# Performance work log

Hardware: AMD Instinct MI355X
Metric: run time of the kernel (lower is better)

The kernel has to match this reference:

```python
import jax, jax.numpy as jnp
import numpy as np

N_EMBD = 1024
NUM_HEADS = 16
HEAD_SIZE = 64


def setup_inputs() -> dict:
    key = jax.random.key(0)
    ks = jax.random.split(key, 6)
    B, T, C, hs = 2, 2048, N_EMBD, HEAD_SIZE
    s = 0.02
    return {
        "x": jax.random.normal(ks[0], (B, T, C), dtype=jnp.float32),
        "Wk": jax.random.normal(ks[1], (hs, C), dtype=jnp.float32) * s,  # torch Linear weight [out,in]
        "Wv": jax.random.normal(ks[2], (hs, C), dtype=jnp.float32) * s,
        "Wq": jax.random.normal(ks[3], (C, C), dtype=jnp.float32) * s,
        "Wp": jax.random.normal(ks[4], (C, C), dtype=jnp.float32) * s,
        "bp": jax.random.normal(ks[5], (C,), dtype=jnp.float32) * s,
    }


def reference(x, Wk, Wv, Wq, Wp, bp):
    B, T, C = x.shape
    H, hs = NUM_HEADS, HEAD_SIZE
    k = x @ Wk.T                      # [B,T,hs]
    v = x @ Wv.T                      # [B,T,hs]
    q = x @ Wq.T                      # [B,T,C]
    # Faithful to torch: raw view of [B,T,C] -> [B,H,T,hs] (row-major reshape, not transpose)
    q = q.reshape(B, H, T, hs)
    k = k.reshape(B, 1, T, hs)
    v = v.reshape(B, 1, T, hs)
    att = jnp.einsum("bhqd,bhkd->bhqk", q, jnp.broadcast_to(k, (B, 1, T, hs))) * (hs ** -0.5)
    mask = jnp.tril(jnp.ones((T, T), dtype=bool))[None, None]  # [1,1,T,T]
    att = jnp.where(mask, att, -jnp.inf)
    att = jax.nn.softmax(att, axis=-1)
    y = jnp.einsum("bhqk,bhkd->bhqd", att, jnp.broadcast_to(v, (B, 1, T, hs)))  # [B,H,T,hs]
    y = jnp.transpose(y, (0, 2, 1, 3)).reshape(B, T, C)
    return y @ Wp.T + bp
```

## Files before the change

kernel.cpp:

```cpp
#include <hip/hip_runtime.h>
#include <cstddef>
#include <cstdint>

#define B_N 2
#define T_N 2048
#define C_N 1024
#define H_N 16
#define HS_N 64
#define M_N (B_N * T_N)

typedef __attribute__((ext_vector_type(8))) short bf16x8;
typedef __attribute__((ext_vector_type(4))) float f32x4;

#define QSCALE 0.18033688011112042f

__device__ __forceinline__ ushort f2bf(float f) {
    union { float f; uint32_t u; } v; v.f = f;
    uint32_t r = v.u + 0x7fffu + ((v.u >> 16) & 1u);
    return (ushort)(r >> 16);
}

#define GLL16(g, l)                                                         \
    __builtin_amdgcn_global_load_lds(                                       \
        (const __attribute__((address_space(1))) unsigned int*)(g),         \
        (__attribute__((address_space(3))) unsigned int*)(l), 16, 0, 0)

__global__ void cvt_all_kernel(const float* __restrict__ x,
                               const float* __restrict__ Wq,
                               const float* __restrict__ Wp,
                               const float* __restrict__ Wk,
                               const float* __restrict__ Wv,
                               ushort* __restrict__ xb,
                               ushort* __restrict__ Wqb,
                               ushort* __restrict__ Wpb,
                               ushort* __restrict__ Wkvb) {
    const int S0 = M_N * C_N / 4;
    const int S1 = S0 + C_N * C_N / 4;
    const int S2 = S1 + C_N * C_N / 4;
    const int S3 = S2 + HS_N * C_N / 4;
    const int S4 = S3 + HS_N * C_N / 4;
    const int stride = gridDim.x * blockDim.x;
    for (int i = blockIdx.x * blockDim.x + threadIdx.x; i < S4; i += stride) {
        const float* src; ushort* dst; int j; float sc = 1.f;
        if (i < S0)      { src = x;  dst = xb;   j = i; }
        else if (i < S1) { src = Wq; dst = Wqb;  j = i - S0; sc = QSCALE; }
        else if (i < S2) { src = Wp; dst = Wpb;  j = i - S1; }
        else if (i < S3) { src = Wk; dst = Wkvb; j = i - S2; }
        else             { src = Wv; dst = Wkvb + HS_N * C_N; j = i - S3; }
        const float4 f = ((const float4*)src)[j];
        ushort4 o;
        o.x = f2bf(f.x * sc); o.y = f2bf(f.y * sc);
        o.z = f2bf(f.z * sc); o.w = f2bf(f.w * sc);
        ((ushort4*)dst)[j] = o;
    }
}

template <int MODE>
__global__ __launch_bounds__(256, 2) void gemm_bf16(
    const ushort* __restrict__ A,
    const ushort* __restrict__ W,
    const float* __restrict__ bias,
    void* __restrict__ Cout,
    ushort* __restrict__ kb,
    ushort* __restrict__ vbt,
    int K)
{
    __shared__ ushort As[64 * 64];
    __shared__ ushort Bs[128 * 64];
    const int m0 = blockIdx.x * 64;
    const int n0 = blockIdx.y * 128;
    const int tid = threadIdx.x;
    const int wid = tid >> 6;
    const int lane = tid & 63;
    const int ln = lane & 15;
    const int quad = lane >> 4;
    const int wm = wid >> 1, wn = wid & 1;

    f32x4 acc[2][4];
    #pragma unroll
    for (int i = 0; i < 2; ++i)
        #pragma unroll
        for (int j = 0; j < 4; ++j)
            acc[i][j] = (f32x4){0.f, 0.f, 0.f, 0.f};

    const int srow = lane >> 3;
    const int schk = (lane & 7) ^ srow;

    for (int k0 = 0; k0 < K; k0 += 64) {
        __syncthreads();
        #pragma unroll
        for (int t = 0; t < 2; ++t) {
            const int seg = wid * 2 + t;
            GLL16(A + (size_t)(m0 + seg * 8 + srow) * K + k0 + schk * 8,
                  As + seg * 512);
        }
        #pragma unroll
        for (int t = 0; t < 4; ++t) {
            const int seg = wid * 4 + t;
            GLL16(W + (size_t)(n0 + seg * 8 + srow) * K + k0 + schk * 8,
                  Bs + seg * 512);
        }
        __syncthreads();

        #pragma unroll
        for (int hh = 0; hh < 2; ++hh) {
            bf16x8 af[2], bf[4];
            const int sw = ln & 7;
            #pragma unroll
            for (int i = 0; i < 2; ++i) {
                const int row = wm * 32 + i * 16 + ln;
                af[i] = *(const bf16x8*)&As[row * 64 + (((hh * 4 + quad) ^ sw) * 8)];
            }
            #pragma unroll
            for (int j = 0; j < 4; ++j) {
                const int row = wn * 64 + j * 16 + ln;
                bf[j] = *(const bf16x8*)&Bs[row * 64 + (((hh * 4 + quad) ^ sw) * 8)];
            }
            #pragma unroll
            for (int i = 0; i < 2; ++i)
                #pragma unroll
                for (int j = 0; j < 4; ++j)
                    acc[i][j] = __builtin_amdgcn_mfma_f32_16x16x32_bf16(
                        af[i], bf[j], acc[i][j], 0, 0, 0);
        }
    }

    if (MODE == 1 && n0 >= C_N) {
        #pragma unroll
        for (int i = 0; i < 2; ++i) {
            const int row0 = m0 + wm * 32 + i * 16 + quad * 4;
            #pragma unroll
            for (int j = 0; j < 4; ++j) {
                const int c2 = wn * 64 + j * 16 + ln;
                if (c2 >= 64) {
                    const int d = c2 - 64;
                    const int b = row0 >> 11;
                    const int t0 = row0 & 2047;
                    ushort4 pk;
                    pk.x = f2bf(acc[i][j][0]); pk.y = f2bf(acc[i][j][1]);
                    pk.z = f2bf(acc[i][j][2]); pk.w = f2bf(acc[i][j][3]);
                    *(ushort4*)&vbt[((size_t)b * 64 + d) * T_N + t0] = pk;
                } else {
                    #pragma unroll
                    for (int reg = 0; reg < 4; ++reg)
                        kb[(size_t)(row0 + reg) * 64 + c2] = f2bf(acc[i][j][reg]);
                }
            }
        }
        return;
    }

    #pragma unroll
    for (int i = 0; i < 2; ++i) {
        #pragma unroll
        for (int j = 0; j < 4; ++j) {
            const int col = n0 + wn * 64 + j * 16 + ln;
            const float bv = (MODE == 0) ? bias[col] : 0.f;
            #pragma unroll
            for (int reg = 0; reg < 4; ++reg) {
                const int row = m0 + wm * 32 + i * 16 + quad * 4 + reg;
                const float v = acc[i][j][reg] + bv;
                if (MODE == 0)
                    ((float*)Cout)[(size_t)row * C_N + col] = v;
                else
                    ((ushort*)Cout)[(size_t)row * C_N + col] = f2bf(v);
            }
        }
    }
}

__global__ __launch_bounds__(256, 2) void attn_mfma_kernel(
    const ushort* __restrict__ qb,
    const ushort* __restrict__ kb,
    const ushort* __restrict__ vbt,
    ushort* __restrict__ yb)
{
    __shared__ ushort Ks[2][64][72];
    __shared__ ushort Vt[2][64][72];
    __shared__ ushort Ps[4][16][72];

    const int bh = blockIdx.x;
    const int b = bh >> 4, h = bh & 15;
    const int p = blockIdx.y;
    const int qA0 = p * 64;
    const int qB0 = (31 - p) * 64;
    const int tid = threadIdx.x;
    const int wid = tid >> 6;
    const int lane = tid & 63;
    const int ln = lane & 15;
    const int quad = lane >> 4;

    const ushort* qstrip = qb + (size_t)b * T_N * C_N + (size_t)h * T_N * HS_N;
    const size_t rB = (size_t)(qB0 + wid * 16 + ln) * HS_N;
    const size_t rA = (size_t)(qA0 + wid * 16 + ln) * HS_N;
    bf16x8 qfB[2], qfA[2];
    qfB[0] = *(const bf16x8*)(qstrip + rB + quad * 8);
    qfB[1] = *(const bf16x8*)(qstrip + rB + 32 + quad * 8);
    qfA[0] = *(const bf16x8*)(qstrip + rA + quad * 8);
    qfA[1] = *(const bf16x8*)(qstrip + rA + 32 + quad * 8);

    f32x4 oB[4], oA[4];
    float lB = 0.f, lA = 0.f;
    #pragma unroll
    for (int nt = 0; nt < 4; ++nt) {
        oB[nt] = (f32x4){0.f, 0.f, 0.f, 0.f};
        oA[nt] = (f32x4){0.f, 0.f, 0.f, 0.f};
    }

    const ushort* kbase = kb + (size_t)b * T_N * HS_N;
    const ushort* vtbase = vbt + (size_t)b * HS_N * T_N;
    const int rs = tid >> 3;
    const int cs = tid & 7;

    const int nkt = 32 - p;

    int4 kc0, kc1, vc0, vc1;
    {
        kc0 = *(const int4*)(kbase + (size_t)rs * HS_N + cs * 8);
        kc1 = *(const int4*)(kbase + (size_t)(rs + 32) * HS_N + cs * 8);
        vc0 = *(const int4*)(vtbase + (size_t)rs * T_N + cs * 8);
        vc1 = *(const int4*)(vtbase + (size_t)(rs + 32) * T_N + cs * 8);
        *(int4*)&Ks[0][rs][cs * 8] = kc0;
        *(int4*)&Ks[0][rs + 32][cs * 8] = kc1;
        *(int4*)&Vt[0][rs][cs * 8] = vc0;
        *(int4*)&Vt[0][rs + 32][cs * 8] = vc1;
    }
    if (nkt > 1) {
        kc0 = *(const int4*)(kbase + (size_t)(64 + rs) * HS_N + cs * 8);
        kc1 = *(const int4*)(kbase + (size_t)(64 + rs + 32) * HS_N + cs * 8);
        vc0 = *(const int4*)(vtbase + (size_t)rs * T_N + 64 + cs * 8);
        vc1 = *(const int4*)(vtbase + (size_t)(rs + 32) * T_N + 64 + cs * 8);
    }
    __syncthreads();

    bf16x8 kf[4][2], vf[4][2];

    auto tile_compute = [&](const bf16x8* qf, f32x4* o, float& l,
                            int qt0, int k0) {
        const int qs0 = qt0 + wid * 16;
        const int qg = qs0 + ln;
        f32x4 sc[4];
        #pragma unroll
        for (int nt = 0; nt < 4; ++nt) {
            sc[nt] = (f32x4){0.f, 0.f, 0.f, 0.f};
            sc[nt] = __builtin_amdgcn_mfma_f32_16x16x32_bf16(
                kf[nt][0], qf[0], sc[nt], 0, 0, 0);
            sc[nt] = __builtin_amdgcn_mfma_f32_16x16x32_bf16(
                kf[nt][1], qf[1], sc[nt], 0, 0, 0);
        }
        const bool dg = (k0 + 63 > qs0);
        #pragma unroll
        for (int nt = 0; nt < 4; ++nt) {
            ushort pk[4];
            #pragma unroll
            for (int reg = 0; reg < 4; ++reg) {
                const int key = k0 + nt * 16 + quad * 4 + reg;
                float sv = sc[nt][reg];
                if (dg && key > qg) sv = -1e30f;
                const float pe = __builtin_amdgcn_exp2f(sv);
                l += pe;
                pk[reg] = f2bf(pe);
            }
            *(uint2*)&Ps[wid][ln][nt * 16 + quad * 4] = *(const uint2*)pk;
        }
        #pragma unroll
        for (int ks2 = 0; ks2 < 2; ++ks2) {
            const bf16x8 pf = *(const bf16x8*)&Ps[wid][ln][ks2 * 32 + quad * 8];
            #pragma unroll
            for (int nt = 0; nt < 4; ++nt)
                o[nt] = __builtin_amdgcn_mfma_f32_16x16x32_bf16(
                    pf, vf[nt][ks2], o[nt], 0, 0, 0);
        }
    };

    for (int kt = 0; kt < nkt; ++kt) {
        const int k0 = kt * 64;
        const int cur = kt & 1, nxt = cur ^ 1;
        if (kt + 1 < nkt) {
            *(int4*)&Ks[nxt][rs][cs * 8] = kc0;
            *(int4*)&Ks[nxt][rs + 32][cs * 8] = kc1;
            *(int4*)&Vt[nxt][rs][cs * 8] = vc0;
            *(int4*)&Vt[nxt][rs + 32][cs * 8] = vc1;
        }
        if (kt + 2 < nkt) {
            const int kn = k0 + 128;
            kc0 = *(const int4*)(kbase + (size_t)(kn + rs) * HS_N + cs * 8);
            kc1 = *(const int4*)(kbase + (size_t)(kn + rs + 32) * HS_N + cs * 8);
            vc0 = *(const int4*)(vtbase + (size_t)rs * T_N + kn + cs * 8);
            vc1 = *(const int4*)(vtbase + (size_t)(rs + 32) * T_N + kn + cs * 8);
        }
        #pragma unroll
        for (int nt = 0; nt < 4; ++nt) {
            kf[nt][0] = *(const bf16x8*)&Ks[cur][nt * 16 + ln][quad * 8];
            kf[nt][1] = *(const bf16x8*)&Ks[cur][nt * 16 + ln][32 + quad * 8];
            vf[nt][0] = *(const bf16x8*)&Vt[cur][nt * 16 + ln][quad * 8];
            vf[nt][1] = *(const bf16x8*)&Vt[cur][nt * 16 + ln][32 + quad * 8];
        }
        tile_compute(qfB, oB, lB, qB0, k0);
        if (kt <= p)
            tile_compute(qfA, oA, lA, qA0, k0);
        __syncthreads();
    }

    #pragma unroll
    for (int t = 0; t < 2; ++t) {
        float l = t ? lA : lB;
        const f32x4* o = t ? oA : oB;
        const int qt0 = t ? qA0 : qB0;
        l += __shfl_xor(l, 16);
        l += __shfl_xor(l, 32);
        #pragma unroll
        for (int reg = 0; reg < 4; ++reg) {
            const float inv = 1.0f / __shfl(l, quad * 4 + reg);
            const int qg = qt0 + wid * 16 + quad * 4 + reg;
            ushort* yrow = yb + (size_t)b * T_N * C_N + (size_t)qg * C_N
                           + h * HS_N;
            #pragma unroll
            for (int nt = 0; nt < 4; ++nt)
                yrow[nt * 16 + ln] = f2bf(o[nt][reg] * inv);
        }
    }
}

extern "C" void kernel_launch(void* const* d_in, const int* in_sizes, int n_in,
                              void* d_out, int out_size, void* d_ws, size_t ws_size,
                              hipStream_t stream) {
    const float* x  = (const float*)d_in[0];
    const float* Wk = (const float*)d_in[1];
    const float* Wv = (const float*)d_in[2];
    const float* Wq = (const float*)d_in[3];
    const float* Wp = (const float*)d_in[4];
    const float* bp = (const float*)d_in[5];
    float* out = (float*)d_out;

    ushort* xb   = (ushort*)d_ws;
    ushort* qb   = xb   + (size_t)M_N * C_N;
    ushort* yb   = qb   + (size_t)M_N * C_N;
    ushort* kbw  = yb   + (size_t)M_N * C_N;
    ushort* vbt  = kbw  + (size_t)M_N * HS_N;
    ushort* Wqb  = vbt  + (size_t)B_N * HS_N * T_N;
    ushort* Wkvb = Wqb  + (size_t)C_N * C_N;
    ushort* Wpb  = Wkvb + (size_t)128 * C_N;

    cvt_all_kernel<<<1024, 256, 0, stream>>>(x, Wq, Wp, Wk, Wv,
                                             xb, Wqb, Wpb, Wkvb);

    gemm_bf16<1><<<dim3(M_N / 64, (C_N + 128) / 128), 256, 0, stream>>>(
        xb, Wqb, nullptr, qb, kbw, vbt, C_N);

    attn_mfma_kernel<<<dim3(B_N * H_N, 16), 256, 0, stream>>>(qb, kbw, vbt, yb);

    gemm_bf16<0><<<dim3(M_N / 64, C_N / 128), 256, 0, stream>>>(
        yb, Wpb, bp, out, nullptr, nullptr, C_N);
}
```

Baseline: 155.1 us.

## Load GEMM and attention MFMA fragments directly from global memory, dropping LDS staging

New measurement: 296.0 us. 90.9% more time.

```diff
diff --git a/kernel.cpp b/kernel.cpp
--- a/kernel.cpp
+++ b/kernel.cpp
@@ -19,11 +19,6 @@
     uint32_t r = v.u + 0x7fffu + ((v.u >> 16) & 1u);
     return (ushort)(r >> 16);
 }
-
-#define GLL16(g, l)                                                         \
-    __builtin_amdgcn_global_load_lds(                                       \
-        (const __attribute__((address_space(1))) unsigned int*)(g),         \
-        (__attribute__((address_space(3))) unsigned int*)(l), 16, 0, 0)
 
 __global__ void cvt_all_kernel(const float* __restrict__ x,
                                const float* __restrict__ Wq,
@@ -55,18 +50,15 @@
     }
 }
 
-template <int MODE>
+template <int MODE, int K>
 __global__ __launch_bounds__(256, 2) void gemm_bf16(
     const ushort* __restrict__ A,
     const ushort* __restrict__ W,
     const float* __restrict__ bias,
     void* __restrict__ Cout,
     ushort* __restrict__ kb,
-    ushort* __restrict__ vbt,
-    int K)
+    ushort* __restrict__ vbt)
 {
-    __shared__ ushort As[64 * 64];
-    __shared__ ushort Bs[128 * 64];
     const int m0 = blockIdx.x * 64;
     const int n0 = blockIdx.y * 128;
     const int tid = threadIdx.x;
@@ -83,46 +75,32 @@
         for (int j = 0; j < 4; ++j)
             acc[i][j] = (f32x4){0.f, 0.f, 0.f, 0.f};
 
-    const int srow = lane >> 3;
-    const int schk = (lane & 7) ^ srow;
-
+    const ushort* Abase = A + (size_t)(m0 + wm * 32 + ln) * K + quad * 8;
+    const ushort* Wbase = W + (size_t)(n0 + wn * 64 + ln) * K + quad * 8;
+
+    #pragma unroll
     for (int k0 = 0; k0 < K; k0 += 64) {
-        __syncthreads();
-        #pragma unroll
-        for (int t = 0; t < 2; ++t) {
-            const int seg = wid * 2 + t;
-            GLL16(A + (size_t)(m0 + seg * 8 + srow) * K + k0 + schk * 8,
-                  As + seg * 512);
-        }
-        #pragma unroll
-        for (int t = 0; t < 4; ++t) {
-            const int seg = wid * 4 + t;
-            GLL16(W + (size_t)(n0 + seg * 8 + srow) * K + k0 + schk * 8,
-                  Bs + seg * 512);
-        }
-        __syncthreads();
-
-        #pragma unroll
-        for (int hh = 0; hh < 2; ++hh) {
-            bf16x8 af[2], bf[4];
-            const int sw = ln & 7;
-            #pragma unroll
-            for (int i = 0; i < 2; ++i) {
-                const int row = wm * 32 + i * 16 + ln;
-                af[i] = *(const bf16x8*)&As[row * 64 + (((hh * 4 + quad) ^ sw) * 8)];
-            }
-            #pragma unroll
-            for (int j = 0; j < 4; ++j) {
-                const int row = wn * 64 + j * 16 + ln;
-                bf[j] = *(const bf16x8*)&Bs[row * 64 + (((hh * 4 + quad) ^ sw) * 8)];
-            }
+        bf16x8 af[2][2], bf[4][2];
+        #pragma unroll
+        for (int i = 0; i < 2; ++i)
+            #pragma unroll
+            for (int hh = 0; hh < 2; ++hh)
+                af[i][hh] = *(const bf16x8*)(Abase + (size_t)i * 16 * K
+                                             + k0 + hh * 32);
+        #pragma unroll
+        for (int j = 0; j < 4; ++j)
+            #pragma unroll
+            for (int hh = 0; hh < 2; ++hh)
+                bf[j][hh] = *(const bf16x8*)(Wbase + (size_t)j * 16 * K
+                                             + k0 + hh * 32);
+        #pragma unroll
+        for (int hh = 0; hh < 2; ++hh)
             #pragma unroll
             for (int i = 0; i < 2; ++i)
                 #pragma unroll
                 for (int j = 0; j < 4; ++j)
                     acc[i][j] = __builtin_amdgcn_mfma_f32_16x16x32_bf16(
-                        af[i], bf[j], acc[i][j], 0, 0, 0);
-        }
+                        af[i][hh], bf[j][hh], acc[i][j], 0, 0, 0);
     }
 
     if (MODE == 1 && n0 >= C_N) {
@@ -175,8 +153,6 @@
     const ushort* __restrict__ vbt,
     ushort* __restrict__ yb)
 {
-    __shared__ ushort Ks[2][64][72];
-    __shared__ ushort Vt[2][64][72];
     __shared__ ushort Ps[4][16][72];
 
     const int bh = blockIdx.x;
@@ -207,33 +183,19 @@
         oA[nt] = (f32x4){0.f, 0.f, 0.f, 0.f};
     }
 
-    const ushort* kbase = kb + (size_t)b * T_N * HS_N;
-    const ushort* vtbase = vbt + (size_t)b * HS_N * T_N;
-    const int rs = tid >> 3;
-    const int cs = tid & 7;
+    const ushort* kfp = kb + (size_t)b * T_N * HS_N + (size_t)ln * HS_N
+                        + quad * 8;
+    const ushort* vfp = vbt + (size_t)b * HS_N * T_N + (size_t)ln * T_N
+                        + quad * 8;
 
     const int nkt = 32 - p;
 
-    int4 kc0, kc1, vc0, vc1;
-    {
-        kc0 = *(const int4*)(kbase + (size_t)rs * HS_N + cs * 8);
-        kc1 = *(const int4*)(kbase + (size_t)(rs + 32) * HS_N + cs * 8);
-        vc0 = *(const int4*)(vtbase + (size_t)rs * T_N + cs * 8);
-        vc1 = *(const int4*)(vtbase + (size_t)(rs + 32) * T_N + cs * 8);
-        *(int4*)&Ks[0][rs][cs * 8] = kc0;
-        *(int4*)&Ks[0][rs + 32][cs * 8] = kc1;
-        *(int4*)&Vt[0][rs][cs * 8] = vc0;
-        *(int4*)&Vt[0][rs + 32][cs * 8] = vc1;
-    }
-    if (nkt > 1) {
-        kc0 = *(const int4*)(kbase + (size_t)(64 + rs) * HS_N + cs * 8);
-        kc1 = *(const int4*)(kbase + (size_t)(64 + rs + 32) * HS_N + cs * 8);
-        vc0 = *(const int4*)(vtbase + (size_t)rs * T_N + 64 + cs * 8);
-        vc1 = *(const int4*)(vtbase + (size_t)(rs + 32) * T_N + 64 + cs * 8);
-    }
-    __syncthreads();
-
-    bf16x8 kf[4][2], vf[4][2];
+    bf16x8 kfc[4][2], kfn[4][2], vf[4][2];
+    #pragma unroll
+    for (int nt = 0; nt < 4; ++nt) {
+        kfc[nt][0] = *(const bf16x8*)(kfp + (size_t)(nt * 16) * HS_N);
+        kfc[nt][1] = *(const bf16x8*)(kfp + (size_t)(nt * 16) * HS_N + 32);
+    }
 
     auto tile_compute = [&](const bf16x8* qf, f32x4* o, float& l,
                             int qt0, int k0) {
@@ -244,9 +206,9 @@
         for (int nt = 0; nt < 4; ++nt) {
             sc[nt] = (f32x4){0.f, 0.f, 0.f, 0.f};
             sc[nt] = __builtin_amdgcn_mfma_f32_16x16x32_bf16(
-                kf[nt][0], qf[0], sc[nt], 0, 0, 0);
+                kfc[nt][0], qf[0], sc[nt], 0, 0, 0);
             sc[nt] = __builtin_amdgcn_mfma_f32_16x16x32_bf16(
-                kf[nt][1], qf[1], sc[nt], 0, 0, 0);
+                kfc[nt][1], qf[1], sc[nt], 0, 0, 0);
         }
         const bool dg = (k0 + 63 > qs0);
         #pragma unroll
@@ -275,31 +237,27 @@
 
     for (int kt = 0; kt < nkt; ++kt) {
         const int k0 = kt * 64;
-        const int cur = kt & 1, nxt = cur ^ 1;
+        #pragma unroll
+        for (int nt = 0; nt < 4; ++nt) {
+            vf[nt][0] = *(const bf16x8*)(vfp + (size_t)(nt * 16) * T_N + k0);
+            vf[nt][1] = *(const bf16x8*)(vfp + (size_t)(nt * 16) * T_N + k0 + 32);
+        }
         if (kt + 1 < nkt) {
-            *(int4*)&Ks[nxt][rs][cs * 8] = kc0;
-            *(int4*)&Ks[nxt][rs + 32][cs * 8] = kc1;
-            *(int4*)&Vt[nxt][rs][cs * 8] = vc0;
-            *(int4*)&Vt[nxt][rs + 32][cs * 8] = vc1;
-        }
-        if (kt + 2 < nkt) {
-            const int kn = k0 + 128;
-            kc0 = *(const int4*)(kbase + (size_t)(kn + rs) * HS_N + cs * 8);
-            kc1 = *(const int4*)(kbase + (size_t)(kn + rs + 32) * HS_N + cs * 8);
-            vc0 = *(const int4*)(vtbase + (size_t)rs * T_N + kn + cs * 8);
-            vc1 = *(const int4*)(vtbase + (size_t)(rs + 32) * T_N + kn + cs * 8);
-        }
-        #pragma unroll
-        for (int nt = 0; nt < 4; ++nt) {
-            kf[nt][0] = *(const bf16x8*)&Ks[cur][nt * 16 + ln][quad * 8];
-            kf[nt][1] = *(const bf16x8*)&Ks[cur][nt * 16 + ln][32 + quad * 8];
-            vf[nt][0] = *(const bf16x8*)&Vt[cur][nt * 16 + ln][quad * 8];
-            vf[nt][1] = *(const bf16x8*)&Vt[cur][nt * 16 + ln][32 + quad * 8];
+            const int kn = k0 + 64;
+            #pragma unroll
+            for (int nt = 0; nt < 4; ++nt) {
+                kfn[nt][0] = *(const bf16x8*)(kfp + (size_t)(kn + nt * 16) * HS_N);
+                kfn[nt][1] = *(const bf16x8*)(kfp + (size_t)(kn + nt * 16) * HS_N + 32);
+            }
         }
         tile_compute(qfB, oB, lB, qB0, k0);
         if (kt <= p)
             tile_compute(qfA, oA, lA, qA0, k0);
-        __syncthreads();
+        #pragma unroll
+        for (int nt = 0; nt < 4; ++nt) {
+            kfc[nt][0] = kfn[nt][0];
+            kfc[nt][1] = kfn[nt][1];
+        }
     }
 
     #pragma unroll
@@ -345,11 +303,11 @@
     cvt_all_kernel<<<1024, 256, 0, stream>>>(x, Wq, Wp, Wk, Wv,
                                              xb, Wqb, Wpb, Wkvb);
 
-    gemm_bf16<1><<<dim3(M_N / 64, (C_N + 128) / 128), 256, 0, stream>>>(
-        xb, Wqb, nullptr, qb, kbw, vbt, C_N);
+    gemm_bf16<1, C_N><<<dim3(M_N / 64, (C_N + 128) / 128), 256, 0, stream>>>(
+        xb, Wqb, nullptr, qb, kbw, vbt);
 
     attn_mfma_kernel<<<dim3(B_N * H_N, 16), 256, 0, stream>>>(qb, kbw, vbt, yb);
 
-    gemm_bf16<0><<<dim3(M_N / 64, C_N / 128), 256, 0, stream>>>(
-        yb, Wpb, bp, out, nullptr, nullptr, C_N);
-}
+    gemm_bf16<0, C_N><<<dim3(M_N / 64, C_N / 128), 256, 0, stream>>>(
+        yb, Wpb, bp, out, nullptr, nullptr);
+}
```
